# Performance work log

Measured on AMD Instinct MI355X. Metric: run time of the kernel, lower is better.

The kernel has to match this reference:

```python
import jax, jax.numpy as jnp
import numpy as np

# Coarse-to-fine lossless 3D segmentation (Seg3dLossless), batch=1, C=1.
RES = [17, 33, 65, 129]          # odd resolutions, stride (RF-1)/(R-1) is integral
RF = RES[-1]
B_MIN, B_MAX = -1.0, 1.0
BAL = 0.5                        # balance_value
N_CONFLICT_ITERS = 2             # fixed unroll of the data-dependent while-loop


def _mlp(pts, w1, b1, w2, b2, w3, b3):
    # query_func: occupancy MLP on normalized (x,y,z) points -> [N]
    h = jax.nn.relu(pts @ w1 + b1)
    h = jax.nn.relu(h @ w2 + b2)
    return jax.nn.sigmoid(h @ w3 + b3)[..., 0]


def _eval_grid(R, w1, b1, w2, b2, w3, b3):
    # batch_eval with align_corners=False: coords2D = (coord + 0.5)/RF, mapped to [B_MIN,B_MAX]
    s = (RF - 1) // (R - 1)
    c = jnp.arange(R, dtype=jnp.float32) * s                 # final-res integer coords
    p = (c + 0.5) / RF * (B_MAX - B_MIN) + B_MIN
    zz, yy, xx = jnp.meshgrid(p, p, p, indexing='ij')        # [D,H,W]
    pts = jnp.stack([xx, yy, zz], axis=-1).reshape(-1, 3)    # (x,y,z) order
    return _mlp(pts, w1, b1, w2, b2, w3, b3).reshape(R, R, R)


def _resize(x, R):
    # trilinear, align_corners=True: out index j -> in coord j*(in-1)/(out-1)
    c = jnp.linspace(0.0, x.shape[0] - 1.0, R)
    zz, yy, xx = jnp.meshgrid(c, c, c, indexing='ij')
    return jax.scipy.ndimage.map_coordinates(x, [zz, yy, xx], order=1, mode='nearest')


def _dilate(m):
    # smooth_conv3x3 (mean filter) followed by >0 == 3x3x3 binary dilation
    f = jax.lax.reduce_window(m.astype(jnp.float32), 0.0, jax.lax.max,
                              (3, 3, 3), (1, 1, 1), 'SAME')
    return f > 0.0


def setup_inputs() -> dict:
    key = jax.random.key(0)
    k1, k2, k3 = jax.random.split(key, 3)
    H = 64
    return {
        'w1': jax.random.normal(k1, (3, H), jnp.float32) * 0.8,
        'b1': jnp.zeros((H,), jnp.float32),
        'w2': jax.random.normal(k2, (H, H), jnp.float32) * (1.0 / np.sqrt(H)),
        'b2': jnp.zeros((H,), jnp.float32),
        'w3': jax.random.normal(k3, (H, 1), jnp.float32) * (1.0 / np.sqrt(H)),
        'b3': jnp.zeros((1,), jnp.float32),
    }


def reference(w1, b1, w2, b2, w3, b3):
    params = (w1, b1, w2, b2, w3, b3)
    # level 0: dense eval on the coarse grid
    occ = _eval_grid(RES[0], *params)                        # [R0,R0,R0]
    s0 = (RF - 1) // (RES[0] - 1)
    calculated = jnp.zeros((RF, RF, RF), bool).at[::s0, ::s0, ::s0].set(True)

    for R in RES[1:]:
        s = (RF - 1) // (R - 1)
        valid = _resize((occ > BAL).astype(jnp.float32), R)  # no-grad mask path
        occ_i = _resize(occ, R)                              # differentiable interp
        boundary = _dilate((valid > 0.0) & (valid < 1.0))
        calc_l = calculated[::s, ::s, ::s]
        boundary = boundary & (~calc_l)                      # skip already-evaluated voxels
        occ_true = _eval_grid(R, *params)                    # query_func at this level
        occ = jnp.where(boundary, occ_true, occ_i)           # scatter of occupancys_topk
        calc_l = calc_l | boundary
        # conflict resolution: re-query 3^3 neighbors of sign-flip voxels
        conflict = boundary & ((occ_i - BAL) * (occ_true - BAL) < 0.0)
        for _ in range(N_CONFLICT_ITERS):
            nbr = _dilate(conflict) & (~calc_l)
            occ_prev = occ
            occ = jnp.where(nbr, occ_true, occ)
            calc_l = calc_l | nbr
            conflict = nbr & ((occ_prev - BAL) * (occ_true - BAL) < 0.0)
        calculated = calculated.at[::s, ::s, ::s].set(calc_l)

    return occ[None, None]                                   # (1, 1, D, H, W)
```

## Files before the change

kernel.cpp:

```cpp
#include <hip/hip_runtime.h>

#define HH 64

static __global__ void k_set_ones(unsigned char* __restrict__ p, int n){
  int i = blockIdx.x * blockDim.x + threadIdx.x;
  if (i < n) p[i] = 1;
}

static __global__ void k_prep_w2t(const float* __restrict__ w2, float* __restrict__ w2t){
  int t = blockIdx.x * 256 + threadIdx.x;
  w2t[t] = w2[(t & 63) * HH + (t >> 6)];
}

__device__ __forceinline__ void mlp_pair(
    const float* __restrict__ sw1,
    const float* __restrict__ sw2t,
    const float* __restrict__ b2, const float* __restrict__ w3,
    const float* __restrict__ b3,
    float xA, float yA, float zA, float xB, float yB, float zB,
    float& outA, float& outB)
{
  const int ibase = ((threadIdx.x & 63) >> 5) * 32;
  float h1a[32], h1b[32];
  #pragma unroll
  for (int k = 0; k < 32; k += 4){
    const float4 wx = *(const float4*)&sw1[      ibase + k];
    const float4 wy = *(const float4*)&sw1[ 64 + ibase + k];
    const float4 wz = *(const float4*)&sw1[128 + ibase + k];
    const float4 bb = *(const float4*)&sw1[192 + ibase + k];
    h1a[k+0] = fmaxf(fmaf(xA,wx.x,fmaf(yA,wy.x,fmaf(zA,wz.x,bb.x))),0.f);
    h1a[k+1] = fmaxf(fmaf(xA,wx.y,fmaf(yA,wy.y,fmaf(zA,wz.y,bb.y))),0.f);
    h1a[k+2] = fmaxf(fmaf(xA,wx.z,fmaf(yA,wy.z,fmaf(zA,wz.z,bb.z))),0.f);
    h1a[k+3] = fmaxf(fmaf(xA,wx.w,fmaf(yA,wy.w,fmaf(zA,wz.w,bb.w))),0.f);
    h1b[k+0] = fmaxf(fmaf(xB,wx.x,fmaf(yB,wy.x,fmaf(zB,wz.x,bb.x))),0.f);
    h1b[k+1] = fmaxf(fmaf(xB,wx.y,fmaf(yB,wy.y,fmaf(zB,wz.y,bb.y))),0.f);
    h1b[k+2] = fmaxf(fmaf(xB,wx.z,fmaf(yB,wy.z,fmaf(zB,wz.z,bb.z))),0.f);
    h1b[k+3] = fmaxf(fmaf(xB,wx.w,fmaf(yB,wy.w,fmaf(zB,wz.w,bb.w))),0.f);
  }
  float oa = b3[0], ob = oa;
  #pragma unroll 1
  for (int j = 0; j < HH; ++j){
    const float4* wrow = (const float4*)&sw2t[j*HH + ibase];
    float a0 = 0.f, a1 = 0.f, c0 = 0.f, c1 = 0.f;
    #pragma unroll
    for (int q = 0; q < 8; q += 2){
      const float4 w0 = wrow[q];
      const float4 w1q = wrow[q+1];
      a0 = fmaf(h1a[4*q+0], w0.x, a0);
      a0 = fmaf(h1a[4*q+1], w0.y, a0);
      a0 = fmaf(h1a[4*q+2], w0.z, a0);
      a0 = fmaf(h1a[4*q+3], w0.w, a0);
      a1 = fmaf(h1a[4*q+4], w1q.x, a1);
      a1 = fmaf(h1a[4*q+5], w1q.y, a1);
      a1 = fmaf(h1a[4*q+6], w1q.z, a1);
      a1 = fmaf(h1a[4*q+7], w1q.w, a1);
      c0 = fmaf(h1b[4*q+0], w0.x, c0);
      c0 = fmaf(h1b[4*q+1], w0.y, c0);
      c0 = fmaf(h1b[4*q+2], w0.z, c0);
      c0 = fmaf(h1b[4*q+3], w0.w, c0);
      c1 = fmaf(h1b[4*q+4], w1q.x, c1);
      c1 = fmaf(h1b[4*q+5], w1q.y, c1);
      c1 = fmaf(h1b[4*q+6], w1q.z, c1);
      c1 = fmaf(h1b[4*q+7], w1q.w, c1);
    }
    float accA = a0 + a1, accB = c0 + c1;
    accA += __shfl_xor(accA, 32);
    accB += __shfl_xor(accB, 32);
    const float bj = b2[j], wj = w3[j];
    oa = fmaf(fmaxf(accA + bj, 0.f), wj, oa);
    ob = fmaf(fmaxf(accB + bj, 0.f), wj, ob);
  }
  outA = 1.f / (1.f + expf(-oa));
  outB = 1.f / (1.f + expf(-ob));
}

#define STAGE_WEIGHTS()                                            \
  __shared__ float sw1[4*HH];                                      \
  __shared__ float sw2t[HH*HH];                                    \
  {                                                                \
    const int t0 = threadIdx.x;                                    \
    if (t0 < 3*HH) sw1[t0] = w1[t0];                               \
    else sw1[t0] = b1[t0 - 3*HH];                                  \
    const float4* s4 = (const float4*)w2t;                         \
    float4* d4 = (float4*)sw2t;                                    \
    for (int i4 = t0; i4 < HH*HH/4; i4 += 256) d4[i4] = s4[i4];    \
    __syncthreads();                                               \
  }

static __global__ __launch_bounds__(256)
__attribute__((amdgpu_waves_per_eu(4,4)))
void k_eval_mlp(
    const float* __restrict__ w1, const float* __restrict__ b1,
    const float* __restrict__ w2t, const float* __restrict__ b2,
    const float* __restrict__ w3, const float* __restrict__ b3,
    float* __restrict__ out, int R, int s)
{
  STAGE_WEIGHTS();
  const unsigned int n = (unsigned int)R * (unsigned int)R * (unsigned int)R;
  const int lane = threadIdx.x & 63;
  const int wid = threadIdx.x >> 6;
  const unsigned int base = blockIdx.x * 256u + (unsigned int)(wid * 64 + (lane & 31));
  const unsigned int pidA = base < n ? base : (n - 1u);
  const unsigned int pB = base + 32u;
  const unsigned int pidB = pB < n ? pB : (n - 1u);
  const float inv129x2 = 2.0f / 129.0f;
  unsigned int cA = pidA % (unsigned int)R, rA = pidA / (unsigned int)R;
  unsigned int cB = pidB % (unsigned int)R, rB = pidB / (unsigned int)R;
  const float xA = ((float)(cA * (unsigned int)s) + 0.5f) * inv129x2 - 1.0f;
  const float yA = ((float)((rA % (unsigned int)R) * (unsigned int)s) + 0.5f) * inv129x2 - 1.0f;
  const float zA = ((float)((rA / (unsigned int)R) * (unsigned int)s) + 0.5f) * inv129x2 - 1.0f;
  const float xB = ((float)(cB * (unsigned int)s) + 0.5f) * inv129x2 - 1.0f;
  const float yB = ((float)((rB % (unsigned int)R) * (unsigned int)s) + 0.5f) * inv129x2 - 1.0f;
  const float zB = ((float)((rB / (unsigned int)R) * (unsigned int)s) + 0.5f) * inv129x2 - 1.0f;
  float oA, oB;
  mlp_pair(sw1, sw2t, b2, w3, b3, xA, yA, zA, xB, yB, zB, oA, oB);
  if ((threadIdx.x & 63) < 32){
    if (base < n) out[pidA] = oA;
    if (pB < n)   out[pidB] = oB;
  }
}

static __global__ __launch_bounds__(256)
__attribute__((amdgpu_waves_per_eu(4,4)))
void k_eval_sparse(
    const float* __restrict__ w1, const float* __restrict__ b1,
    const float* __restrict__ w2t, const float* __restrict__ b2,
    const float* __restrict__ w3, const float* __restrict__ b3,
    const int* __restrict__ idxl, const unsigned int* __restrict__ cnt,
    const float* __restrict__ occ_i,
    float* __restrict__ out, unsigned char* __restrict__ mism,
    int R, int s, unsigned int n)
{
  unsigned int count = *cnt;
  if (count > n) count = n;
  if (blockIdx.x * 256u >= count) return;
  STAGE_WEIGHTS();
  const int lane = threadIdx.x & 63;
  const int wid = threadIdx.x >> 6;
  const unsigned int slotA = blockIdx.x * 256u + (unsigned int)(wid * 64 + (lane & 31));
  const unsigned int slotB = slotA + 32u;
  const bool vA = slotA < count, vB = slotB < count;
  const unsigned int pidA = (unsigned int)idxl[vA ? slotA : 0];
  const unsigned int pidB = (unsigned int)idxl[vB ? slotB : 0];
  const float inv129x2 = 2.0f / 129.0f;
  unsigned int cA = pidA % (unsigned int)R, rA = pidA / (unsigned int)R;
  unsigned int cB = pidB % (unsigned int)R, rB = pidB / (unsigned int)R;
  const float xA = ((float)(cA * (unsigned int)s) + 0.5f) * inv129x2 - 1.0f;
  const float yA = ((float)((rA % (unsigned int)R) * (unsigned int)s) + 0.5f) * inv129x2 - 1.0f;
  const float zA = ((float)((rA / (unsigned int)R) * (unsigned int)s) + 0.5f) * inv129x2 - 1.0f;
  const float xB = ((float)(cB * (unsigned int)s) + 0.5f) * inv129x2 - 1.0f;
  const float yB = ((float)((rB % (unsigned int)R) * (unsigned int)s) + 0.5f) * inv129x2 - 1.0f;
  const float zB = ((float)((rB / (unsigned int)R) * (unsigned int)s) + 0.5f) * inv129x2 - 1.0f;
  float oA, oB;
  mlp_pair(sw1, sw2t, b2, w3, b3, xA, yA, zA, xB, yB, zB, oA, oB);
  if ((threadIdx.x & 63) < 32){
    if (vA){
      out[pidA] = oA;
      mism[pidA] = ((occ_i[pidA] - 0.5f) * (oA - 0.5f) < 0.0f) ? (unsigned char)1 : (unsigned char)0;
    }
    if (vB){
      out[pidB] = oB;
      mism[pidB] = ((occ_i[pidB] - 0.5f) * (oB - 0.5f) < 0.0f) ? (unsigned char)1 : (unsigned char)0;
    }
  }
}

static __global__ __launch_bounds__(256) void k_resize_b0(
    const float* __restrict__ prev,
    const unsigned char* __restrict__ calc_prev,
    float* __restrict__ occ_i, float* __restrict__ occ_out,
    unsigned char* __restrict__ bnd0, unsigned char* __restrict__ calc_out,
    unsigned char* __restrict__ confA, unsigned char* __restrict__ confB,
    unsigned char* __restrict__ upd, int R, int Rp)
{
  const unsigned int n = (unsigned int)R * (unsigned int)R * (unsigned int)R;
  unsigned int gid = blockIdx.x * 256u + threadIdx.x;
  if (gid >= n) return;
  int c = (int)(gid % (unsigned int)R);
  unsigned int r = gid / (unsigned int)R;
  int b = (int)(r % (unsigned int)R);
  int a = (int)(r / (unsigned int)R);
  int a0 = a >> 1, da = a & 1;
  int b0i = b >> 1, db = b & 1;
  int c0 = c >> 1, dc = c & 1;
  float sum = 0.0f;
  int cnt = 0;
  const int tot = (da + 1) * (db + 1) * (dc + 1);
  for (int dz = 0; dz <= da; ++dz)
    for (int dy = 0; dy <= db; ++dy)
      for (int dx = 0; dx <= dc; ++dx){
        float v = prev[((unsigned int)(a0 + dz) * (unsigned int)Rp + (unsigned int)(b0i + dy)) * (unsigned int)Rp + (unsigned int)(c0 + dx)];
        sum += v;
        cnt += (v > 0.5f) ? 1 : 0;
      }
  float oi = sum / (float)tot;
  occ_i[gid] = oi;
  occ_out[gid] = oi;
  bnd0[gid] = (cnt > 0 && cnt < tot) ? 1 : 0;
  calc_out[gid] = ((da | db | dc) == 0)
      ? calc_prev[((unsigned int)a0 * (unsigned int)Rp + (unsigned int)b0i) * (unsigned int)Rp + (unsigned int)c0]
      : (unsigned char)0;
  confA[gid] = 0; confB[gid] = 0; upd[gid] = 0;
}

static __global__ __launch_bounds__(256) void k_resize_boundary(
    const float* __restrict__ prev, const float* __restrict__ occ_true,
    const unsigned char* __restrict__ calc_prev,
    float* __restrict__ occ_i, float* __restrict__ occ_out,
    unsigned char* __restrict__ bnd0,
    unsigned char* __restrict__ mism, unsigned char* __restrict__ calc_out,
    int R, int Rp)
{
  const unsigned int n = (unsigned int)R * (unsigned int)R * (unsigned int)R;
  unsigned int gid = blockIdx.x * 256u + threadIdx.x;
  if (gid >= n) return;
  int c = (int)(gid % (unsigned int)R);
  unsigned int r = gid / (unsigned int)R;
  int b = (int)(r % (unsigned int)R);
  int a = (int)(r / (unsigned int)R);
  int a0 = a >> 1, da = a & 1;
  int b0i = b >> 1, db = b & 1;
  int c0 = c >> 1, dc = c & 1;
  float sum = 0.0f;
  int cnt = 0;
  const int tot = (da + 1) * (db + 1) * (dc + 1);
  for (int dz = 0; dz <= da; ++dz)
    for (int dy = 0; dy <= db; ++dy)
      for (int dx = 0; dx <= dc; ++dx){
        float v = prev[((unsigned int)(a0 + dz) * (unsigned int)Rp + (unsigned int)(b0i + dy)) * (unsigned int)Rp + (unsigned int)(c0 + dx)];
        sum += v;
        cnt += (v > 0.5f) ? 1 : 0;
      }
  float oi = sum / (float)tot;
  occ_i[gid] = oi;
  occ_out[gid] = oi;
  bnd0[gid] = (cnt > 0 && cnt < tot) ? 1 : 0;
  mism[gid] = ((oi - 0.5f) * (occ_true[gid] - 0.5f) < 0.0f) ? 1 : 0;
  calc_out[gid] = ((da | db | dc) == 0)
      ? calc_prev[((unsigned int)a0 * (unsigned int)Rp + (unsigned int)b0i) * (unsigned int)Rp + (unsigned int)c0]
      : (unsigned char)0;
}

static __global__ __launch_bounds__(256) void k_dil7x(
    const unsigned char* __restrict__ in, unsigned char* __restrict__ outp, int R)
{
  const unsigned int n = (unsigned int)R * (unsigned int)R * (unsigned int)R;
  unsigned int gid = blockIdx.x * 256u + threadIdx.x;
  if (gid >= n) return;
  int c = (int)(gid % (unsigned int)R);
  int g = (int)gid;
  int m = 0;
  #pragma unroll
  for (int d = -3; d <= 3; ++d){
    int q = c + d;
    if (q >= 0 && q < R) m |= in[g + d];
  }
  outp[gid] = (unsigned char)(m ? 1 : 0);
}

static __global__ __launch_bounds__(256) void k_dil7y(
    const unsigned char* __restrict__ in, unsigned char* __restrict__ outp, int R)
{
  const unsigned int n = (unsigned int)R * (unsigned int)R * (unsigned int)R;
  unsigned int gid = blockIdx.x * 256u + threadIdx.x;
  if (gid >= n) return;
  unsigned int r = gid / (unsigned int)R;
  int b = (int)(r % (unsigned int)R);
  int g = (int)gid;
  int m = 0;
  #pragma unroll
  for (int d = -3; d <= 3; ++d){
    int q = b + d;
    if (q >= 0 && q < R) m |= in[g + d * R];
  }
  outp[gid] = (unsigned char)(m ? 1 : 0);
}

static __global__ __launch_bounds__(256) void k_dil7z_count(
    const unsigned char* __restrict__ in, unsigned char* __restrict__ outp,
    unsigned int* __restrict__ bcnt, int R)
{
  const unsigned int n = (unsigned int)R * (unsigned int)R * (unsigned int)R;
  unsigned int gid = blockIdx.x * 256u + threadIdx.x;
  int m = 0;
  if (gid < n){
    int a = (int)(gid / ((unsigned int)R * (unsigned int)R));
    int g = (int)gid;
    int RR = R * R;
    #pragma unroll
    for (int d = -3; d <= 3; ++d){
      int q = a + d;
      if (q >= 0 && q < R) m |= in[g + d * RR];
    }
    outp[gid] = (unsigned char)(m ? 1 : 0);
  }
  unsigned long long bm = __ballot(m != 0);
  __shared__ unsigned int wc[4];
  int wid = (int)(threadIdx.x >> 6);
  if ((threadIdx.x & 63u) == 0) wc[wid] = (unsigned int)__popcll(bm);
  __syncthreads();
  if (threadIdx.x == 0) bcnt[blockIdx.x] = wc[0] + wc[1] + wc[2] + wc[3];
}

static __global__ __launch_bounds__(1024) void k_scan(
    unsigned int* __restrict__ bcnt, unsigned int nb, unsigned int* __restrict__ total)
{
  __shared__ unsigned int part[1024];
  const unsigned int t = threadIdx.x;
  const unsigned int chunk = (nb + 1023u) / 1024u;
  const unsigned int beg = t * chunk;
  const unsigned int end = (beg + chunk < nb) ? (beg + chunk) : nb;
  unsigned int s = 0;
  for (unsigned int i = beg; i < end; ++i) s += bcnt[i];
  part[t] = s;
  __syncthreads();
  for (int offd = 1; offd < 1024; offd <<= 1){
    unsigned int v = (t >= (unsigned int)offd) ? part[t - offd] : 0u;
    __syncthreads();
    part[t] += v;
    __syncthreads();
  }
  unsigned int run = (t == 0) ? 0u : part[t - 1];
  for (unsigned int i = beg; i < end; ++i){
    unsigned int v = bcnt[i];
    bcnt[i] = run;
    run += v;
  }
  if (t == 1023) *total = part[1023];
}

static __global__ __launch_bounds__(256) void k_scatter(
    const unsigned char* __restrict__ cand, const unsigned int* __restrict__ boff,
    int* __restrict__ idxl, unsigned int n)
{
  unsigned int gid = blockIdx.x * 256u + threadIdx.x;
  bool pred = (gid < n) && (cand[gid] != 0);
  unsigned long long m = __ballot(pred);
  __shared__ unsigned int wbase[4];
  int wid = (int)(threadIdx.x >> 6);
  int lane = (int)(threadIdx.x & 63u);
  if (lane == 0) wbase[wid] = (unsigned int)__popcll(m);
  __syncthreads();
  if (threadIdx.x == 0){
    unsigned int b = boff[blockIdx.x];
    unsigned int t0 = wbase[0], t1 = wbase[1], t2 = wbase[2];
    wbase[0] = b; wbase[1] = b + t0; wbase[2] = b + t0 + t1; wbase[3] = b + t0 + t1 + t2;
  }
  __syncthreads();
  if (pred){
    int pre = __popcll(m & ((1ull << lane) - 1ull));
    idxl[wbase[wid] + (unsigned int)pre] = (int)gid;
  }
}

static __global__ __launch_bounds__(256) void k_dilate_sparse(
    const int* __restrict__ idxl, const unsigned int* __restrict__ cnt,
    const unsigned char* __restrict__ src, const unsigned char* __restrict__ mism,
    unsigned char* __restrict__ calc, unsigned char* __restrict__ conf_out,
    unsigned char* __restrict__ upd, int R, int final_step,
    const float* __restrict__ occ_true, float* __restrict__ occ_out,
    unsigned int n)
{
  unsigned int count = *cnt;
  if (count > n) count = n;
  for (unsigned int slot = blockIdx.x * 256u + threadIdx.x; slot < count;
       slot += gridDim.x * 256u){
    int gid = idxl[slot];
    int c = gid % R;
    int r = gid / R;
    int b = r % R;
    int a = r / R;
    int m = 0;
    for (int dz = -1; dz <= 1; ++dz){
      int az = a + dz; if (az < 0 || az >= R) continue;
      for (int dy = -1; dy <= 1; ++dy){
        int by = b + dy; if (by < 0 || by >= R) continue;
        for (int dx = -1; dx <= 1; ++dx){
          int cx = c + dx; if (cx < 0 || cx >= R) continue;
          m |= src[(az * R + by) * R + cx];
        }
      }
    }
    unsigned char nb = (m && !calc[gid]) ? (unsigned char)1 : (unsigned char)0;
    conf_out[gid] = (nb && mism[gid]) ? (unsigned char)1 : (unsigned char)0;
    unsigned char u = upd[gid];
    if (nb){ calc[gid] = 1; if (!u){ upd[gid] = 1; u = 1; } }
    if (final_step && u) occ_out[gid] = occ_true[gid];
  }
}

static __global__ __launch_bounds__(256) void k_dilate_step(
    const unsigned char* __restrict__ src, const unsigned char* __restrict__ mism,
    unsigned char* __restrict__ calc, unsigned char* __restrict__ conf_out,
    unsigned char* __restrict__ upd, int R, int first, int final_step,
    const float* __restrict__ occ_true, float* __restrict__ occ_out)
{
  const unsigned int n = (unsigned int)R * (unsigned int)R * (unsigned int)R;
  unsigned int gid = blockIdx.x * 256u + threadIdx.x;
  if (gid >= n) return;
  int c = (int)(gid % (unsigned int)R);
  unsigned int r = gid / (unsigned int)R;
  int b = (int)(r % (unsigned int)R);
  int a = (int)(r / (unsigned int)R);
  int m = 0;
  for (int dz = -1; dz <= 1; ++dz){
    int az = a + dz; if (az < 0 || az >= R) continue;
    for (int dy = -1; dy <= 1; ++dy){
      int by = b + dy; if (by < 0 || by >= R) continue;
      for (int dx = -1; dx <= 1; ++dx){
        int cx = c + dx; if (cx < 0 || cx >= R) continue;
        m |= src[((unsigned int)az * (unsigned int)R + (unsigned int)by) * (unsigned int)R + (unsigned int)cx];
      }
    }
  }
  unsigned char nb = (m && !calc[gid]) ? (unsigned char)1 : (unsigned char)0;
  if (nb) calc[gid] = 1;
  conf_out[gid] = (nb && mism[gid]) ? (unsigned char)1 : (unsigned char)0;
  unsigned char u;
  if (first){ u = nb; upd[gid] = nb; }
  else { u = upd[gid]; if (nb && !u){ upd[gid] = 1; u = 1; } }
  if (final_step && u) occ_out[gid] = occ_true[gid];
}

extern "C" void kernel_launch(void* const* d_in, const int* in_sizes, int n_in,
                              void* d_out, int out_size, void* d_ws, size_t ws_size,
                              hipStream_t stream)
{
  const float* w1 = (const float*)d_in[0];
  const float* b1 = (const float*)d_in[1];
  const float* w2 = (const float*)d_in[2];
  const float* b2 = (const float*)d_in[3];
  const float* w3 = (const float*)d_in[4];
  const float* b3 = (const float*)d_in[5];
  float* out = (float*)d_out;

  const int NF = 129 * 129 * 129;
  const int NP = 65 * 65 * 65;
  char* ws = (char*)d_ws;
  size_t off = 0;
  auto alloc = [&](size_t bytes) -> void* {
    void* p = (void*)(ws + off);
    off += (bytes + 255) & ~(size_t)255;
    return p;
  };
  float* f_true  = (float*)alloc((size_t)NF * 4);
  float* f_occi  = (float*)alloc((size_t)NF * 4);
  float* f_prevA = (float*)alloc((size_t)NP * 4);
  float* f_prevB = (float*)alloc((size_t)NP * 4);
  float* f_w2t   = (float*)alloc((size_t)HH * HH * 4);
  int*   i_idx   = (int*)alloc((size_t)NF * 4);
  unsigned int* u_cnt  = (unsigned int*)alloc(256);
  unsigned int* u_bcnt = (unsigned int*)alloc(8448 * 4);
  unsigned char* b_b0    = (unsigned char*)alloc(NF);
  unsigned char* b_mism  = (unsigned char*)alloc(NF);
  unsigned char* b_confA = (unsigned char*)alloc(NF);
  unsigned char* b_confB = (unsigned char*)alloc(NF);
  unsigned char* b_calcA = (unsigned char*)alloc(NF);
  unsigned char* b_calcB = (unsigned char*)alloc(NF);
  unsigned char* b_upd   = (unsigned char*)alloc(NF);
  unsigned char* b_cand  = (unsigned char*)alloc(NF);
  unsigned char* b_tmp   = (unsigned char*)alloc(NF);
  (void)ws_size;

  k_prep_w2t<<<16, 256, 0, stream>>>(w2, f_w2t);

  {
    int R = 17, s = 8;
    int n = R * R * R;
    int blocks = (n + 255) / 256;
    k_eval_mlp<<<blocks, 256, 0, stream>>>(w1, b1, f_w2t, b2, w3, b3, f_prevA, R, s);
    k_set_ones<<<blocks, 256, 0, stream>>>(b_calcA, n);
  }

  int Rp = 17;
  float* prev = f_prevA;
  unsigned char* calcP = b_calcA;
  unsigned char* calcC = b_calcB;
  for (int li = 1; li <= 3; ++li){
    int R = 2 * Rp - 1;
    int s = 128 / (R - 1);
    unsigned int n = (unsigned int)R * (unsigned int)R * (unsigned int)R;
    int blocks = (int)((n + 255u) / 256u);
    float* occ_out = (li == 3) ? out : ((prev == f_prevA) ? f_prevB : f_prevA);

    if (R == 33){
      k_eval_mlp<<<blocks, 256, 0, stream>>>(w1, b1, f_w2t, b2, w3, b3, f_true, R, s);
      k_resize_boundary<<<blocks, 256, 0, stream>>>(prev, f_true, calcP, f_occi, occ_out, b_b0, b_mism, calcC, R, Rp);
      k_dilate_step<<<blocks, 256, 0, stream>>>(b_b0,    b_mism, calcC, b_confA, b_upd, R, 1, 0, f_true, occ_out);
      k_dilate_step<<<blocks, 256, 0, stream>>>(b_confA, b_mism, calcC, b_confB, b_upd, R, 0, 0, f_true, occ_out);
      k_dilate_step<<<blocks, 256, 0, stream>>>(b_confB, b_mism, calcC, b_confA, b_upd, R, 0, 1, f_true, occ_out);
    } else {
      k_resize_b0<<<blocks, 256, 0, stream>>>(prev, calcP, f_occi, occ_out, b_b0, calcC,
                                              b_confA, b_confB, b_upd, R, Rp);
      k_dil7x<<<blocks, 256, 0, stream>>>(b_b0,  b_tmp,  R);
      k_dil7y<<<blocks, 256, 0, stream>>>(b_tmp, b_cand, R);
      k_dil7z_count<<<blocks, 256, 0, stream>>>(b_cand, b_tmp, u_bcnt, R);
      k_scan<<<1, 1024, 0, stream>>>(u_bcnt, (unsigned int)blocks, u_cnt);
      k_scatter<<<blocks, 256, 0, stream>>>(b_tmp, u_bcnt, i_idx, n);
      k_eval_sparse<<<blocks, 256, 0, stream>>>(
          w1, b1, f_w2t, b2, w3, b3, i_idx, u_cnt, f_occi, f_true, b_mism, R, s, n);
      int sblocks = blocks < 4096 ? blocks : 4096;
      k_dilate_sparse<<<sblocks, 256, 0, stream>>>(i_idx, u_cnt, b_b0,    b_mism, calcC, b_confA, b_upd, R, 0, f_true, occ_out, n);
      k_dilate_sparse<<<sblocks, 256, 0, stream>>>(i_idx, u_cnt, b_confA, b_mism, calcC, b_confB, b_upd, R, 0, f_true, occ_out, n);
      k_dilate_sparse<<<sblocks, 256, 0, stream>>>(i_idx, u_cnt, b_confB, b_mism, calcC, b_confA, b_upd, R, 1, f_true, occ_out, n);
    }

    prev = occ_out;
    unsigned char* tmpc = calcP; calcP = calcC; calcC = tmpc;
    Rp = R;
  }
  (void)in_sizes; (void)n_in; (void)out_size;
}
```

Measured before the change: 307.4 us.

## Fuse pipeline kernels and replace scan-based compaction with atomic wave compaction

Cuts the launch count in several ways. The level-17 eval is fused with the calc-flag init, and the level-33 dense eval with resize/boundary. The x and y dilation passes are merged into one 2D pass. The block-count/scan/scatter compaction becomes per-wave atomicAdd into a counter that resize_b0 resets. The sparse MLP eval is fused with the first conflict dilation step. Output order of the compacted index list becomes nondeterministic, and the merged 7x7 xy pass does more reads per voxel.

```diff
diff --git a/kernel.cpp b/kernel.cpp
--- a/kernel.cpp
+++ b/kernel.cpp
@@ -1,11 +1,6 @@
 #include <hip/hip_runtime.h>
 
 #define HH 64
-
-static __global__ void k_set_ones(unsigned char* __restrict__ p, int n){
-  int i = blockIdx.x * blockDim.x + threadIdx.x;
-  if (i < n) p[i] = 1;
-}
 
 static __global__ void k_prep_w2t(const float* __restrict__ w2, float* __restrict__ w2t){
   int t = blockIdx.x * 256 + threadIdx.x;
@@ -13,8 +8,8 @@
 }
 
 __device__ __forceinline__ void mlp_pair(
-    const float* __restrict__ sw1,
-    const float* __restrict__ sw2t,
+    const float* sw1,
+    const float* sw2t,
     const float* __restrict__ b2, const float* __restrict__ w3,
     const float* __restrict__ b3,
     float xA, float yA, float zA, float xB, float yB, float zB,
@@ -74,6 +69,15 @@
   outB = 1.f / (1.f + expf(-ob));
 }
 
+__device__ __forceinline__ void pid2xyz(unsigned int pid, int R, int s,
+                                        float& x, float& y, float& z){
+  const float inv129x2 = 2.0f / 129.0f;
+  unsigned int c = pid % (unsigned int)R, r = pid / (unsigned int)R;
+  x = ((float)(c * (unsigned int)s) + 0.5f) * inv129x2 - 1.0f;
+  y = ((float)((r % (unsigned int)R) * (unsigned int)s) + 0.5f) * inv129x2 - 1.0f;
+  z = ((float)((r / (unsigned int)R) * (unsigned int)s) + 0.5f) * inv129x2 - 1.0f;
+}
+
 #define STAGE_WEIGHTS()                                            \
   __shared__ float sw1[4*HH];                                      \
   __shared__ float sw2t[HH*HH];                                    \
@@ -89,79 +93,85 @@
 
 static __global__ __launch_bounds__(256)
 __attribute__((amdgpu_waves_per_eu(4,4)))
-void k_eval_mlp(
+void k_eval17(
     const float* __restrict__ w1, const float* __restrict__ b1,
     const float* __restrict__ w2t, const float* __restrict__ b2,
     const float* __restrict__ w3, const float* __restrict__ b3,
-    float* __restrict__ out, int R, int s)
+    float* __restrict__ out, unsigned char* __restrict__ calc)
 {
   STAGE_WEIGHTS();
-  const unsigned int n = (unsigned int)R * (unsigned int)R * (unsigned int)R;
+  const int R = 17, s = 8;
+  const unsigned int n = 17u * 17u * 17u;
   const int lane = threadIdx.x & 63;
   const int wid = threadIdx.x >> 6;
   const unsigned int base = blockIdx.x * 256u + (unsigned int)(wid * 64 + (lane & 31));
+  const unsigned int myb = (lane < 32) ? base : base + 32u;
   const unsigned int pidA = base < n ? base : (n - 1u);
   const unsigned int pB = base + 32u;
   const unsigned int pidB = pB < n ? pB : (n - 1u);
-  const float inv129x2 = 2.0f / 129.0f;
-  unsigned int cA = pidA % (unsigned int)R, rA = pidA / (unsigned int)R;
-  unsigned int cB = pidB % (unsigned int)R, rB = pidB / (unsigned int)R;
-  const float xA = ((float)(cA * (unsigned int)s) + 0.5f) * inv129x2 - 1.0f;
-  const float yA = ((float)((rA % (unsigned int)R) * (unsigned int)s) + 0.5f) * inv129x2 - 1.0f;
-  const float zA = ((float)((rA / (unsigned int)R) * (unsigned int)s) + 0.5f) * inv129x2 - 1.0f;
-  const float xB = ((float)(cB * (unsigned int)s) + 0.5f) * inv129x2 - 1.0f;
-  const float yB = ((float)((rB % (unsigned int)R) * (unsigned int)s) + 0.5f) * inv129x2 - 1.0f;
-  const float zB = ((float)((rB / (unsigned int)R) * (unsigned int)s) + 0.5f) * inv129x2 - 1.0f;
-  float oA, oB;
-  mlp_pair(sw1, sw2t, b2, w3, b3, xA, yA, zA, xB, yB, zB, oA, oB);
-  if ((threadIdx.x & 63) < 32){
-    if (base < n) out[pidA] = oA;
-    if (pB < n)   out[pidB] = oB;
-  }
+  float xA,yA,zA,xB,yB,zB, oA,oB;
+  pid2xyz(pidA, R, s, xA, yA, zA);
+  pid2xyz(pidB, R, s, xB, yB, zB);
+  mlp_pair(sw1, sw2t, b2, w3, b3, xA,yA,zA, xB,yB,zB, oA, oB);
+  const unsigned int my_pid = (lane < 32) ? pidA : pidB;
+  const float my_o = (lane < 32) ? oA : oB;
+  if (myb < n){ out[my_pid] = my_o; calc[my_pid] = 1; }
 }
 
 static __global__ __launch_bounds__(256)
 __attribute__((amdgpu_waves_per_eu(4,4)))
-void k_eval_sparse(
+void k_eval_resize33(
     const float* __restrict__ w1, const float* __restrict__ b1,
     const float* __restrict__ w2t, const float* __restrict__ b2,
     const float* __restrict__ w3, const float* __restrict__ b3,
-    const int* __restrict__ idxl, const unsigned int* __restrict__ cnt,
-    const float* __restrict__ occ_i,
-    float* __restrict__ out, unsigned char* __restrict__ mism,
-    int R, int s, unsigned int n)
-{
-  unsigned int count = *cnt;
-  if (count > n) count = n;
-  if (blockIdx.x * 256u >= count) return;
+    const float* __restrict__ prev, const unsigned char* __restrict__ calc_prev,
+    float* __restrict__ occ_i, float* __restrict__ occ_out,
+    unsigned char* __restrict__ bnd0, unsigned char* __restrict__ mism,
+    unsigned char* __restrict__ calc_out, float* __restrict__ f_true)
+{
   STAGE_WEIGHTS();
+  const int R = 33, s = 4, Rp = 17;
+  const unsigned int n = 33u * 33u * 33u;
   const int lane = threadIdx.x & 63;
   const int wid = threadIdx.x >> 6;
-  const unsigned int slotA = blockIdx.x * 256u + (unsigned int)(wid * 64 + (lane & 31));
-  const unsigned int slotB = slotA + 32u;
-  const bool vA = slotA < count, vB = slotB < count;
-  const unsigned int pidA = (unsigned int)idxl[vA ? slotA : 0];
-  const unsigned int pidB = (unsigned int)idxl[vB ? slotB : 0];
-  const float inv129x2 = 2.0f / 129.0f;
-  unsigned int cA = pidA % (unsigned int)R, rA = pidA / (unsigned int)R;
-  unsigned int cB = pidB % (unsigned int)R, rB = pidB / (unsigned int)R;
-  const float xA = ((float)(cA * (unsigned int)s) + 0.5f) * inv129x2 - 1.0f;
-  const float yA = ((float)((rA % (unsigned int)R) * (unsigned int)s) + 0.5f) * inv129x2 - 1.0f;
-  const float zA = ((float)((rA / (unsigned int)R) * (unsigned int)s) + 0.5f) * inv129x2 - 1.0f;
-  const float xB = ((float)(cB * (unsigned int)s) + 0.5f) * inv129x2 - 1.0f;
-  const float yB = ((float)((rB % (unsigned int)R) * (unsigned int)s) + 0.5f) * inv129x2 - 1.0f;
-  const float zB = ((float)((rB / (unsigned int)R) * (unsigned int)s) + 0.5f) * inv129x2 - 1.0f;
-  float oA, oB;
-  mlp_pair(sw1, sw2t, b2, w3, b3, xA, yA, zA, xB, yB, zB, oA, oB);
-  if ((threadIdx.x & 63) < 32){
-    if (vA){
-      out[pidA] = oA;
-      mism[pidA] = ((occ_i[pidA] - 0.5f) * (oA - 0.5f) < 0.0f) ? (unsigned char)1 : (unsigned char)0;
-    }
-    if (vB){
-      out[pidB] = oB;
-      mism[pidB] = ((occ_i[pidB] - 0.5f) * (oB - 0.5f) < 0.0f) ? (unsigned char)1 : (unsigned char)0;
-    }
+  const unsigned int base = blockIdx.x * 256u + (unsigned int)(wid * 64 + (lane & 31));
+  const unsigned int myb = (lane < 32) ? base : base + 32u;
+  const unsigned int pidA = base < n ? base : (n - 1u);
+  const unsigned int pB = base + 32u;
+  const unsigned int pidB = pB < n ? pB : (n - 1u);
+  float xA,yA,zA,xB,yB,zB, oA,oB;
+  pid2xyz(pidA, R, s, xA, yA, zA);
+  pid2xyz(pidB, R, s, xB, yB, zB);
+  mlp_pair(sw1, sw2t, b2, w3, b3, xA,yA,zA, xB,yB,zB, oA, oB);
+  const unsigned int gid = (lane < 32) ? pidA : pidB;
+  const float my_o = (lane < 32) ? oA : oB;
+  if (myb < n){
+    f_true[gid] = my_o;
+    int c = (int)(gid % (unsigned int)R);
+    unsigned int r = gid / (unsigned int)R;
+    int b = (int)(r % (unsigned int)R);
+    int a = (int)(r / (unsigned int)R);
+    int a0 = a >> 1, da = a & 1;
+    int b0i = b >> 1, db = b & 1;
+    int c0 = c >> 1, dc = c & 1;
+    float sum = 0.0f;
+    int cnt = 0;
+    const int tot = (da + 1) * (db + 1) * (dc + 1);
+    for (int dz = 0; dz <= da; ++dz)
+      for (int dy = 0; dy <= db; ++dy)
+        for (int dx = 0; dx <= dc; ++dx){
+          float v = prev[((unsigned int)(a0 + dz) * (unsigned int)Rp + (unsigned int)(b0i + dy)) * (unsigned int)Rp + (unsigned int)(c0 + dx)];
+          sum += v;
+          cnt += (v > 0.5f) ? 1 : 0;
+        }
+    float oi = sum / (float)tot;
+    occ_i[gid] = oi;
+    occ_out[gid] = oi;
+    bnd0[gid] = (cnt > 0 && cnt < tot) ? 1 : 0;
+    mism[gid] = ((oi - 0.5f) * (my_o - 0.5f) < 0.0f) ? 1 : 0;
+    calc_out[gid] = ((da | db | dc) == 0)
+        ? calc_prev[((unsigned int)a0 * (unsigned int)Rp + (unsigned int)b0i) * (unsigned int)Rp + (unsigned int)c0]
+        : (unsigned char)0;
   }
 }
 
@@ -171,10 +181,12 @@
     float* __restrict__ occ_i, float* __restrict__ occ_out,
     unsigned char* __restrict__ bnd0, unsigned char* __restrict__ calc_out,
     unsigned char* __restrict__ confA, unsigned char* __restrict__ confB,
-    unsigned char* __restrict__ upd, int R, int Rp)
+    unsigned char* __restrict__ upd, unsigned int* __restrict__ u_cnt,
+    int R, int Rp)
 {
   const unsigned int n = (unsigned int)R * (unsigned int)R * (unsigned int)R;
   unsigned int gid = blockIdx.x * 256u + threadIdx.x;
+  if (gid == 0) *u_cnt = 0u;
   if (gid >= n) return;
   int c = (int)(gid % (unsigned int)R);
   unsigned int r = gid / (unsigned int)R;
@@ -203,13 +215,8 @@
   confA[gid] = 0; confB[gid] = 0; upd[gid] = 0;
 }
 
-static __global__ __launch_bounds__(256) void k_resize_boundary(
-    const float* __restrict__ prev, const float* __restrict__ occ_true,
-    const unsigned char* __restrict__ calc_prev,
-    float* __restrict__ occ_i, float* __restrict__ occ_out,
-    unsigned char* __restrict__ bnd0,
-    unsigned char* __restrict__ mism, unsigned char* __restrict__ calc_out,
-    int R, int Rp)
+static __global__ __launch_bounds__(256) void k_dil7xy(
+    const unsigned char* __restrict__ in, unsigned char* __restrict__ outp, int R)
 {
   const unsigned int n = (unsigned int)R * (unsigned int)R * (unsigned int)R;
   unsigned int gid = blockIdx.x * 256u + threadIdx.x;
@@ -217,68 +224,25 @@
   int c = (int)(gid % (unsigned int)R);
   unsigned int r = gid / (unsigned int)R;
   int b = (int)(r % (unsigned int)R);
-  int a = (int)(r / (unsigned int)R);
-  int a0 = a >> 1, da = a & 1;
-  int b0i = b >> 1, db = b & 1;
-  int c0 = c >> 1, dc = c & 1;
-  float sum = 0.0f;
-  int cnt = 0;
-  const int tot = (da + 1) * (db + 1) * (dc + 1);
-  for (int dz = 0; dz <= da; ++dz)
-    for (int dy = 0; dy <= db; ++dy)
-      for (int dx = 0; dx <= dc; ++dx){
-        float v = prev[((unsigned int)(a0 + dz) * (unsigned int)Rp + (unsigned int)(b0i + dy)) * (unsigned int)Rp + (unsigned int)(c0 + dx)];
-        sum += v;
-        cnt += (v > 0.5f) ? 1 : 0;
-      }
-  float oi = sum / (float)tot;
-  occ_i[gid] = oi;
-  occ_out[gid] = oi;
-  bnd0[gid] = (cnt > 0 && cnt < tot) ? 1 : 0;
-  mism[gid] = ((oi - 0.5f) * (occ_true[gid] - 0.5f) < 0.0f) ? 1 : 0;
-  calc_out[gid] = ((da | db | dc) == 0)
-      ? calc_prev[((unsigned int)a0 * (unsigned int)Rp + (unsigned int)b0i) * (unsigned int)Rp + (unsigned int)c0]
-      : (unsigned char)0;
-}
-
-static __global__ __launch_bounds__(256) void k_dil7x(
-    const unsigned char* __restrict__ in, unsigned char* __restrict__ outp, int R)
-{
-  const unsigned int n = (unsigned int)R * (unsigned int)R * (unsigned int)R;
-  unsigned int gid = blockIdx.x * 256u + threadIdx.x;
-  if (gid >= n) return;
-  int c = (int)(gid % (unsigned int)R);
   int g = (int)gid;
   int m = 0;
   #pragma unroll
-  for (int d = -3; d <= 3; ++d){
-    int q = c + d;
-    if (q >= 0 && q < R) m |= in[g + d];
+  for (int dy = -3; dy <= 3; ++dy){
+    int qy = b + dy;
+    if (qy < 0 || qy >= R) continue;
+    const unsigned char* row = in + g + dy * R;
+    #pragma unroll
+    for (int dx = -3; dx <= 3; ++dx){
+      int qx = c + dx;
+      if (qx >= 0 && qx < R) m |= row[dx];
+    }
   }
   outp[gid] = (unsigned char)(m ? 1 : 0);
 }
 
-static __global__ __launch_bounds__(256) void k_dil7y(
-    const unsigned char* __restrict__ in, unsigned char* __restrict__ outp, int R)
-{
-  const unsigned int n = (unsigned int)R * (unsigned int)R * (unsigned int)R;
-  unsigned int gid = blockIdx.x * 256u + threadIdx.x;
-  if (gid >= n) return;
-  unsigned int r = gid / (unsigned int)R;
-  int b = (int)(r % (unsigned int)R);
-  int g = (int)gid;
-  int m = 0;
-  #pragma unroll
-  for (int d = -3; d <= 3; ++d){
-    int q = b + d;
-    if (q >= 0 && q < R) m |= in[g + d * R];
-  }
-  outp[gid] = (unsigned char)(m ? 1 : 0);
-}
-
-static __global__ __launch_bounds__(256) void k_dil7z_count(
-    const unsigned char* __restrict__ in, unsigned char* __restrict__ outp,
-    unsigned int* __restrict__ bcnt, int R)
+static __global__ __launch_bounds__(256) void k_dil7z_scat(
+    const unsigned char* __restrict__ in, int* __restrict__ idxl,
+    unsigned int* __restrict__ u_cnt, int R)
 {
   const unsigned int n = (unsigned int)R * (unsigned int)R * (unsigned int)R;
   unsigned int gid = blockIdx.x * 256u + threadIdx.x;
@@ -292,64 +256,70 @@
       int q = a + d;
       if (q >= 0 && q < R) m |= in[g + d * RR];
     }
-    outp[gid] = (unsigned char)(m ? 1 : 0);
-  }
+  }
+  int lane = (int)(threadIdx.x & 63u);
   unsigned long long bm = __ballot(m != 0);
-  __shared__ unsigned int wc[4];
-  int wid = (int)(threadIdx.x >> 6);
-  if ((threadIdx.x & 63u) == 0) wc[wid] = (unsigned int)__popcll(bm);
-  __syncthreads();
-  if (threadIdx.x == 0) bcnt[blockIdx.x] = wc[0] + wc[1] + wc[2] + wc[3];
-}
-
-static __global__ __launch_bounds__(1024) void k_scan(
-    unsigned int* __restrict__ bcnt, unsigned int nb, unsigned int* __restrict__ total)
-{
-  __shared__ unsigned int part[1024];
-  const unsigned int t = threadIdx.x;
-  const unsigned int chunk = (nb + 1023u) / 1024u;
-  const unsigned int beg = t * chunk;
-  const unsigned int end = (beg + chunk < nb) ? (beg + chunk) : nb;
-  unsigned int s = 0;
-  for (unsigned int i = beg; i < end; ++i) s += bcnt[i];
-  part[t] = s;
-  __syncthreads();
-  for (int offd = 1; offd < 1024; offd <<= 1){
-    unsigned int v = (t >= (unsigned int)offd) ? part[t - offd] : 0u;
-    __syncthreads();
-    part[t] += v;
-    __syncthreads();
-  }
-  unsigned int run = (t == 0) ? 0u : part[t - 1];
-  for (unsigned int i = beg; i < end; ++i){
-    unsigned int v = bcnt[i];
-    bcnt[i] = run;
-    run += v;
-  }
-  if (t == 1023) *total = part[1023];
-}
-
-static __global__ __launch_bounds__(256) void k_scatter(
-    const unsigned char* __restrict__ cand, const unsigned int* __restrict__ boff,
-    int* __restrict__ idxl, unsigned int n)
-{
-  unsigned int gid = blockIdx.x * 256u + threadIdx.x;
-  bool pred = (gid < n) && (cand[gid] != 0);
-  unsigned long long m = __ballot(pred);
-  __shared__ unsigned int wbase[4];
-  int wid = (int)(threadIdx.x >> 6);
-  int lane = (int)(threadIdx.x & 63u);
-  if (lane == 0) wbase[wid] = (unsigned int)__popcll(m);
-  __syncthreads();
-  if (threadIdx.x == 0){
-    unsigned int b = boff[blockIdx.x];
-    unsigned int t0 = wbase[0], t1 = wbase[1], t2 = wbase[2];
-    wbase[0] = b; wbase[1] = b + t0; wbase[2] = b + t0 + t1; wbase[3] = b + t0 + t1 + t2;
-  }
-  __syncthreads();
-  if (pred){
-    int pre = __popcll(m & ((1ull << lane) - 1ull));
-    idxl[wbase[wid] + (unsigned int)pre] = (int)gid;
+  unsigned int wbase = 0;
+  if (lane == 0 && bm) wbase = atomicAdd(u_cnt, (unsigned int)__popcll(bm));
+  wbase = __shfl(wbase, 0);
+  if (m) idxl[wbase + (unsigned int)__popcll(bm & ((1ull << lane) - 1ull))] = (int)gid;
+}
+
+static __global__ __launch_bounds__(256)
+__attribute__((amdgpu_waves_per_eu(4,4)))
+void k_eval_dil1(
+    const float* __restrict__ w1, const float* __restrict__ b1,
+    const float* __restrict__ w2t, const float* __restrict__ b2,
+    const float* __restrict__ w3, const float* __restrict__ b3,
+    const int* __restrict__ idxl, const unsigned int* __restrict__ cnt,
+    const float* __restrict__ occ_i,
+    float* __restrict__ f_true, unsigned char* __restrict__ mism,
+    const unsigned char* __restrict__ b0, unsigned char* __restrict__ calc,
+    unsigned char* __restrict__ conf_out, unsigned char* __restrict__ upd,
+    int R, int s, unsigned int n)
+{
+  unsigned int count = *cnt;
+  if (count > n) count = n;
+  if (blockIdx.x * 256u >= count) return;
+  STAGE_WEIGHTS();
+  const int lane = threadIdx.x & 63;
+  const int wid = threadIdx.x >> 6;
+  const unsigned int slotA = blockIdx.x * 256u + (unsigned int)(wid * 64 + (lane & 31));
+  const unsigned int slotB = slotA + 32u;
+  const bool vA = slotA < count, vB = slotB < count;
+  const unsigned int pidA = (unsigned int)idxl[vA ? slotA : 0];
+  const unsigned int pidB = (unsigned int)idxl[vB ? slotB : 0];
+  float xA,yA,zA,xB,yB,zB, oA,oB;
+  pid2xyz(pidA, R, s, xA, yA, zA);
+  pid2xyz(pidB, R, s, xB, yB, zB);
+  mlp_pair(sw1, sw2t, b2, w3, b3, xA,yA,zA, xB,yB,zB, oA, oB);
+  const bool my_v = (lane < 32) ? vA : vB;
+  const unsigned int my_pid = (lane < 32) ? pidA : pidB;
+  const float my_o = (lane < 32) ? oA : oB;
+  if (my_v){
+    f_true[my_pid] = my_o;
+    const float oi = occ_i[my_pid];
+    const unsigned char mm = ((oi - 0.5f) * (my_o - 0.5f) < 0.0f) ? (unsigned char)1 : (unsigned char)0;
+    mism[my_pid] = mm;
+    int gid = (int)my_pid;
+    int c = gid % R;
+    int r = gid / R;
+    int b = r % R;
+    int a = r / R;
+    int m = 0;
+    for (int dz = -1; dz <= 1; ++dz){
+      int az = a + dz; if (az < 0 || az >= R) continue;
+      for (int dy = -1; dy <= 1; ++dy){
+        int by = b + dy; if (by < 0 || by >= R) continue;
+        for (int dx = -1; dx <= 1; ++dx){
+          int cx = c + dx; if (cx < 0 || cx >= R) continue;
+          m |= b0[(az * R + by) * R + cx];
+        }
+      }
+    }
+    unsigned char nb = (m && !calc[gid]) ? (unsigned char)1 : (unsigned char)0;
+    conf_out[gid] = (nb && mm) ? (unsigned char)1 : (unsigned char)0;
+    if (nb){ calc[gid] = 1; upd[gid] = 1; }
   }
 }
 
@@ -449,8 +419,7 @@
   float* f_prevB = (float*)alloc((size_t)NP * 4);
   float* f_w2t   = (float*)alloc((size_t)HH * HH * 4);
   int*   i_idx   = (int*)alloc((size_t)NF * 4);
-  unsigned int* u_cnt  = (unsigned int*)alloc(256);
-  unsigned int* u_bcnt = (unsigned int*)alloc(8448 * 4);
+  unsigned int* u_cnt = (unsigned int*)alloc(256);
   unsigned char* b_b0    = (unsigned char*)alloc(NF);
   unsigned char* b_mism  = (unsigned char*)alloc(NF);
   unsigned char* b_confA = (unsigned char*)alloc(NF);
@@ -459,55 +428,54 @@
   unsigned char* b_calcB = (unsigned char*)alloc(NF);
   unsigned char* b_upd   = (unsigned char*)alloc(NF);
   unsigned char* b_cand  = (unsigned char*)alloc(NF);
-  unsigned char* b_tmp   = (unsigned char*)alloc(NF);
   (void)ws_size;
 
   k_prep_w2t<<<16, 256, 0, stream>>>(w2, f_w2t);
 
+  k_eval17<<<20, 256, 0, stream>>>(w1, b1, f_w2t, b2, w3, b3, f_prevA, b_calcA);
+
   {
-    int R = 17, s = 8;
-    int n = R * R * R;
-    int blocks = (n + 255) / 256;
-    k_eval_mlp<<<blocks, 256, 0, stream>>>(w1, b1, f_w2t, b2, w3, b3, f_prevA, R, s);
-    k_set_ones<<<blocks, 256, 0, stream>>>(b_calcA, n);
-  }
-
-  int Rp = 17;
-  float* prev = f_prevA;
-  unsigned char* calcP = b_calcA;
-  unsigned char* calcC = b_calcB;
-  for (int li = 1; li <= 3; ++li){
-    int R = 2 * Rp - 1;
-    int s = 128 / (R - 1);
-    unsigned int n = (unsigned int)R * (unsigned int)R * (unsigned int)R;
-    int blocks = (int)((n + 255u) / 256u);
-    float* occ_out = (li == 3) ? out : ((prev == f_prevA) ? f_prevB : f_prevA);
-
-    if (R == 33){
-      k_eval_mlp<<<blocks, 256, 0, stream>>>(w1, b1, f_w2t, b2, w3, b3, f_true, R, s);
-      k_resize_boundary<<<blocks, 256, 0, stream>>>(prev, f_true, calcP, f_occi, occ_out, b_b0, b_mism, calcC, R, Rp);
-      k_dilate_step<<<blocks, 256, 0, stream>>>(b_b0,    b_mism, calcC, b_confA, b_upd, R, 1, 0, f_true, occ_out);
-      k_dilate_step<<<blocks, 256, 0, stream>>>(b_confA, b_mism, calcC, b_confB, b_upd, R, 0, 0, f_true, occ_out);
-      k_dilate_step<<<blocks, 256, 0, stream>>>(b_confB, b_mism, calcC, b_confA, b_upd, R, 0, 1, f_true, occ_out);
-    } else {
-      k_resize_b0<<<blocks, 256, 0, stream>>>(prev, calcP, f_occi, occ_out, b_b0, calcC,
-                                              b_confA, b_confB, b_upd, R, Rp);
-      k_dil7x<<<blocks, 256, 0, stream>>>(b_b0,  b_tmp,  R);
-      k_dil7y<<<blocks, 256, 0, stream>>>(b_tmp, b_cand, R);
-      k_dil7z_count<<<blocks, 256, 0, stream>>>(b_cand, b_tmp, u_bcnt, R);
-      k_scan<<<1, 1024, 0, stream>>>(u_bcnt, (unsigned int)blocks, u_cnt);
-      k_scatter<<<blocks, 256, 0, stream>>>(b_tmp, u_bcnt, i_idx, n);
-      k_eval_sparse<<<blocks, 256, 0, stream>>>(
-          w1, b1, f_w2t, b2, w3, b3, i_idx, u_cnt, f_occi, f_true, b_mism, R, s, n);
-      int sblocks = blocks < 4096 ? blocks : 4096;
-      k_dilate_sparse<<<sblocks, 256, 0, stream>>>(i_idx, u_cnt, b_b0,    b_mism, calcC, b_confA, b_upd, R, 0, f_true, occ_out, n);
-      k_dilate_sparse<<<sblocks, 256, 0, stream>>>(i_idx, u_cnt, b_confA, b_mism, calcC, b_confB, b_upd, R, 0, f_true, occ_out, n);
-      k_dilate_sparse<<<sblocks, 256, 0, stream>>>(i_idx, u_cnt, b_confB, b_mism, calcC, b_confA, b_upd, R, 1, f_true, occ_out, n);
-    }
-
-    prev = occ_out;
-    unsigned char* tmpc = calcP; calcP = calcC; calcC = tmpc;
-    Rp = R;
-  }
+    const int R = 33;
+    const int blocks = (33*33*33 + 255) / 256;
+    k_eval_resize33<<<blocks, 256, 0, stream>>>(
+        w1, b1, f_w2t, b2, w3, b3,
+        f_prevA, b_calcA, f_occi, f_prevB, b_b0, b_mism, b_calcB, f_true);
+    k_dilate_step<<<blocks, 256, 0, stream>>>(b_b0,    b_mism, b_calcB, b_confA, b_upd, R, 1, 0, f_true, f_prevB);
+    k_dilate_step<<<blocks, 256, 0, stream>>>(b_confA, b_mism, b_calcB, b_confB, b_upd, R, 0, 0, f_true, f_prevB);
+    k_dilate_step<<<blocks, 256, 0, stream>>>(b_confB, b_mism, b_calcB, b_confA, b_upd, R, 0, 1, f_true, f_prevB);
+  }
+
+  {
+    const int R = 65, s = 2, Rp = 33;
+    const unsigned int n = 65u*65u*65u;
+    const int blocks = (int)((n + 255u) / 256u);
+    const int sblocks = blocks < 4096 ? blocks : 4096;
+    k_resize_b0<<<blocks, 256, 0, stream>>>(f_prevB, b_calcB, f_occi, f_prevA, b_b0, b_calcA,
+                                            b_confA, b_confB, b_upd, u_cnt, R, Rp);
+    k_dil7xy<<<blocks, 256, 0, stream>>>(b_b0, b_cand, R);
+    k_dil7z_scat<<<blocks, 256, 0, stream>>>(b_cand, i_idx, u_cnt, R);
+    k_eval_dil1<<<blocks, 256, 0, stream>>>(
+        w1, b1, f_w2t, b2, w3, b3, i_idx, u_cnt, f_occi,
+        f_true, b_mism, b_b0, b_calcA, b_confA, b_upd, R, s, n);
+    k_dilate_sparse<<<sblocks, 256, 0, stream>>>(i_idx, u_cnt, b_confA, b_mism, b_calcA, b_confB, b_upd, R, 0, f_true, f_prevA, n);
+    k_dilate_sparse<<<sblocks, 256, 0, stream>>>(i_idx, u_cnt, b_confB, b_mism, b_calcA, b_confA, b_upd, R, 1, f_true, f_prevA, n);
+  }
+
+  {
+    const int R = 129, s = 1, Rp = 65;
+    const unsigned int n = 129u*129u*129u;
+    const int blocks = (int)((n + 255u) / 256u);
+    const int sblocks = blocks < 4096 ? blocks : 4096;
+    k_resize_b0<<<blocks, 256, 0, stream>>>(f_prevA, b_calcA, f_occi, out, b_b0, b_calcB,
+                                            b_confA, b_confB, b_upd, u_cnt, R, Rp);
+    k_dil7xy<<<blocks, 256, 0, stream>>>(b_b0, b_cand, R);
+    k_dil7z_scat<<<blocks, 256, 0, stream>>>(b_cand, i_idx, u_cnt, R);
+    k_eval_dil1<<<blocks, 256, 0, stream>>>(
+        w1, b1, f_w2t, b2, w3, b3, i_idx, u_cnt, f_occi,
+        f_true, b_mism, b_b0, b_calcB, b_confA, b_upd, R, s, n);
+    k_dilate_sparse<<<sblocks, 256, 0, stream>>>(i_idx, u_cnt, b_confA, b_mism, b_calcB, b_confB, b_upd, R, 0, f_true, out, n);
+    k_dilate_sparse<<<sblocks, 256, 0, stream>>>(i_idx, u_cnt, b_confB, b_mism, b_calcB, b_confA, b_upd, R, 1, f_true, out, n);
+  }
+
   (void)in_sizes; (void)n_in; (void)out_size;
 }
```

Result: slower. 511.0 us (+66.2%).
